# Optimization experiments

Measured on AMD Instinct MI355X. Metric: run time of the kernel, lower is better.

Reference implementation:

```python
import jax, jax.numpy as jnp
import numpy as np

B, M, N, L = 4096, 128, 96, 20


def setup_inputs() -> dict:
    key = jax.random.key(0)
    k1, k2, k3, k4 = jax.random.split(key, 4)
    x_ini = jax.random.normal(k1, (B, N, 1), jnp.float32)
    y = jax.random.normal(k2, (B, M, 1), jnp.float32)
    H = jax.random.normal(k3, (B, M, N), jnp.float32)
    xt = jax.random.normal(k4, (B, N, 1), jnp.float32)
    # learned parameters, initialized exactly as in the torch __init__
    grad_ss = jnp.full((L,), 0.001, jnp.float32)
    extra = []
    t = 1.0
    for _ in range(L):
        t1 = (1.0 + np.sqrt(1.0 + 4.0 * t * t)) / 2.0
        extra.append((t - 1.0) / t1)
        t = t1
    extra_ss = jnp.asarray(np.array(extra, dtype=np.float32))
    gamma1 = jnp.asarray(np.array([(5.0 - 0.1) / L * i + 0.1 for i in range(L)], dtype=np.float32))
    return {"x_ini": x_ini, "y": y, "H": H, "xt": xt,
            "grad_ss": grad_ss, "extra_ss": extra_ss, "gamma1": gamma1}


def reference(x_ini, y, H, xt, grad_ss, extra_ss, gamma1):
    central = jnp.array([-2.0, 0.0, 2.0], dtype=x_ini.dtype)  # 3-point codebook
    HTH = jnp.einsum('bmn,bmk->bnk', H, H)   # [B,N,N]
    HTy = jnp.einsum('bmn,bmk->bnk', H, y)   # [B,N,1]

    def step(carry, params):
        x, y_x = carry
        gs, es, gm = params
        grad_f = 2.0 * (jnp.matmul(HTH, y_x) - HTy)          # [B,N,1]
        x_buff = y_x - gs * grad_f                            # [B,N,1]
        # nearest-center lookup over the 3-entry codebook
        idx = jnp.argmin(jnp.abs(x_buff - central[None, None, :]), axis=2)  # [B,N]
        center = central[idx][..., None]                      # [B,N,1]
        ply = 2.0 * jax.nn.sigmoid(gm * (x_buff - center)) - 1.0
        y_x_new = ply + es * (ply - x)                        # FISTA momentum
        return (ply, y_x_new), None

    (x, _), _ = jax.lax.scan(step, (x_ini, x_ini), (grad_ss, extra_ss, gamma1))
    d = x - xt
    loss = jnp.sum(d * d).reshape(1, 1)  # sum_b (x-xt)^T (x-xt)
    return x, loss
```

## Files before the change

kernel.cpp:

```cpp
#include <hip/hip_runtime.h>

#define NB 4096
#define MM 128
#define NN 96
#define LL 20

typedef __attribute__((ext_vector_type(8))) short bf16x8;
typedef __attribute__((ext_vector_type(4))) float f32x4;
typedef __attribute__((ext_vector_type(4))) unsigned int u32x4;

#define HTP_STRIDE  67
#define HTHP_STRIDE 100
#define U_WORDS     (NN * HTHP_STRIDE)

#define SEL_HI 0x07060302u
#define SEL_LO 0x05040100u

__device__ __forceinline__ unsigned bf16_rne(float f) {
    unsigned u = __float_as_uint(f);
    return (u + 0x7fffu + ((u >> 16) & 1u)) >> 16;
}
__device__ __forceinline__ unsigned pack_hl(float v) {
    unsigned hi = bf16_rne(v);
    unsigned lo = bf16_rne(v - __uint_as_float(hi << 16));
    return (hi << 16) | (lo & 0xffffu);
}
__device__ __forceinline__ bf16x8 mk8(unsigned a, unsigned b, unsigned c, unsigned d) {
    u32x4 t; t[0] = a; t[1] = b; t[2] = c; t[3] = d;
    return __builtin_bit_cast(bf16x8, t);
}
struct PairHL { bf16x8 hi, lo; };
__device__ __forceinline__ PairHL build_pair(const unsigned q[8]) {
    PairHL p;
    p.hi = mk8(__builtin_amdgcn_perm(q[1], q[0], SEL_HI), __builtin_amdgcn_perm(q[3], q[2], SEL_HI),
               __builtin_amdgcn_perm(q[5], q[4], SEL_HI), __builtin_amdgcn_perm(q[7], q[6], SEL_HI));
    p.lo = mk8(__builtin_amdgcn_perm(q[1], q[0], SEL_LO), __builtin_amdgcn_perm(q[3], q[2], SEL_LO),
               __builtin_amdgcn_perm(q[5], q[4], SEL_LO), __builtin_amdgcn_perm(q[7], q[6], SEL_LO));
    return p;
}

__global__ __launch_bounds__(256) __attribute__((amdgpu_waves_per_eu(4)))
void pg_kernel(const float* __restrict__ x_ini,
               const float* __restrict__ y,
               const float* __restrict__ H,
               const float* __restrict__ xt,
               const float* __restrict__ grad_ss,
               const float* __restrict__ extra_ss,
               const float* __restrict__ gamma1,
               float* __restrict__ out)
{
    __shared__ __align__(16) unsigned U[U_WORDS];
    __shared__ __align__(16) unsigned yxP[NN];
    __shared__ __align__(16) float wbuf[NN];
    __shared__ float pgs[LL], pes[LL], pgm[LL];
    __shared__ float lsum[4];

    const int b    = blockIdx.x;
    const int tid  = threadIdx.x;
    const int lane = tid & 63;
    const int wid  = tid >> 6;
    const int m15  = lane & 15;
    const int g4   = lane >> 4;

    if (tid < LL) { pgs[tid] = grad_ss[tid]; pes[tid] = extra_ss[tid]; pgm[tid] = gamma1[tid]; }

    const int nJ = (wid == 3) ? 1 : 2;
    f32x4 acc[2][6];
    #pragma unroll
    for (int j = 0; j < 2; ++j)
        #pragma unroll
        for (int i = 0; i < 6; ++i)
            #pragma unroll
            for (int r = 0; r < 4; ++r) acc[j][i][r] = 0.f;

    const float* Hb = H + (size_t)b * (MM * NN);
    const int r16 = tid >> 2;
    const int cg4 = tid & 3;

    for (int kh = 0; kh < 2; ++kh) {
        if (kh) __syncthreads();
        {
            const float* src = Hb + (size_t)(kh * 64 + r16) * NN + cg4 * 24;
            float4 vv[6];
            #pragma unroll
            for (int i = 0; i < 6; ++i) vv[i] = *(const float4*)(src + 4 * i);
            #pragma unroll
            for (int i = 0; i < 6; ++i) {
                const int c = cg4 * 24 + 4 * i;
                U[(c + 0) * HTP_STRIDE + r16] = pack_hl(vv[i].x);
                U[(c + 1) * HTP_STRIDE + r16] = pack_hl(vv[i].y);
                U[(c + 2) * HTP_STRIDE + r16] = pack_hl(vv[i].z);
                U[(c + 3) * HTP_STRIDE + r16] = pack_hl(vv[i].w);
            }
            if (tid < 64)
                U[96 * HTP_STRIDE + tid] = pack_hl(y[(size_t)b * MM + kh * 64 + tid]);
        }
        __syncthreads();

        #pragma unroll
        for (int kk = 0; kk < 2; ++kk) {
            const int kbase = kk * 32 + g4 * 8;
            PairHL B[2];
            #pragma unroll
            for (int j = 0; j < 2; ++j) {
                if (j < nJ) {
                    const int J = wid + 4 * j;
                    unsigned q[8];
                    const unsigned* p = &U[(J * 16 + m15) * HTP_STRIDE + kbase];
                    #pragma unroll
                    for (int u = 0; u < 8; ++u) q[u] = p[u];
                    B[j] = build_pair(q);
                }
            }
            #pragma unroll
            for (int I = 0; I < 6; ++I) {
                unsigned q[8];
                const unsigned* p = &U[(I * 16 + m15) * HTP_STRIDE + kbase];
                #pragma unroll
                for (int u = 0; u < 8; ++u) q[u] = p[u];
                PairHL A = build_pair(q);
                #pragma unroll
                for (int j = 0; j < 2; ++j) {
                    if (j < nJ) {
                        acc[j][I] = __builtin_amdgcn_mfma_f32_16x16x32_bf16(A.hi, B[j].hi, acc[j][I], 0, 0, 0);
                        acc[j][I] = __builtin_amdgcn_mfma_f32_16x16x32_bf16(A.hi, B[j].lo, acc[j][I], 0, 0, 0);
                        acc[j][I] = __builtin_amdgcn_mfma_f32_16x16x32_bf16(A.lo, B[j].hi, acc[j][I], 0, 0, 0);
                    }
                }
            }
        }
    }
    __syncthreads();

    #pragma unroll
    for (int j = 0; j < 2; ++j) {
        if (j < nJ) {
            const int col = (wid + 4 * j) * 16 + m15;
            if (col <= 96) {
                #pragma unroll
                for (int I = 0; I < 6; ++I) {
                    const int rowb = I * 16 + g4 * 4;
                    #pragma unroll
                    for (int r = 0; r < 4; ++r)
                        U[(rowb + r) * HTHP_STRIDE + col] = pack_hl(acc[j][I][r]);
                }
            }
        }
    }
    __syncthreads();

    float yx_own = 0.f, x_c = 0.f, hty = 0.f;
    if (tid < NN) {
        yx_own = x_ini[(size_t)b * NN + tid];
        x_c    = yx_own;
        yxP[tid] = pack_hl(yx_own);
        unsigned p = U[tid * HTHP_STRIDE + 96];
        hty = __uint_as_float(p & 0xffff0000u) + __uint_as_float(p << 16);
    }
    const int nI = (wid < 2) ? 2 : 1;
    bf16x8 ahi[2][3], alo[2][3];
    #pragma unroll
    for (int t2 = 0; t2 < 2; ++t2) {
        if (t2 < nI) {
            const int I = wid + 4 * t2;
            #pragma unroll
            for (int kk = 0; kk < 3; ++kk) {
                unsigned q[8];
                const unsigned* p = &U[(I * 16 + m15) * HTHP_STRIDE + kk * 32 + g4 * 8];
                #pragma unroll
                for (int u = 0; u < 8; ++u) q[u] = p[u];
                PairHL A = build_pair(q);
                ahi[t2][kk] = A.hi;
                alo[t2][kk] = A.lo;
            }
        }
    }
    __syncthreads();

    for (int t = 0; t < LL; ++t) {
        bf16x8 bhi[3], blo[3];
        #pragma unroll
        for (int kk = 0; kk < 3; ++kk) {
            unsigned q[8];
            const unsigned* p = &yxP[kk * 32 + g4 * 8];
            #pragma unroll
            for (int u = 0; u < 8; ++u) q[u] = p[u];
            PairHL Bp = build_pair(q);
            bhi[kk] = Bp.hi; blo[kk] = Bp.lo;
        }
        f32x4 a0 = {0.f,0.f,0.f,0.f}, a1 = {0.f,0.f,0.f,0.f};
        #pragma unroll
        for (int kk = 0; kk < 3; ++kk) {
            a0 = __builtin_amdgcn_mfma_f32_16x16x32_bf16(ahi[0][kk], bhi[kk], a0, 0, 0, 0);
            a0 = __builtin_amdgcn_mfma_f32_16x16x32_bf16(ahi[0][kk], blo[kk], a0, 0, 0, 0);
            a0 = __builtin_amdgcn_mfma_f32_16x16x32_bf16(alo[0][kk], bhi[kk], a0, 0, 0, 0);
            if (1 < nI) {
                a1 = __builtin_amdgcn_mfma_f32_16x16x32_bf16(ahi[1][kk], bhi[kk], a1, 0, 0, 0);
                a1 = __builtin_amdgcn_mfma_f32_16x16x32_bf16(ahi[1][kk], blo[kk], a1, 0, 0, 0);
                a1 = __builtin_amdgcn_mfma_f32_16x16x32_bf16(alo[1][kk], bhi[kk], a1, 0, 0, 0);
            }
        }
        if (m15 == 0) {
            const int rb0 = wid * 16 + g4 * 4;
            wbuf[rb0 + 0] = a0[0]; wbuf[rb0 + 1] = a0[1];
            wbuf[rb0 + 2] = a0[2]; wbuf[rb0 + 3] = a0[3];
            if (1 < nI) {
                const int rb1 = (wid + 4) * 16 + g4 * 4;
                wbuf[rb1 + 0] = a1[0]; wbuf[rb1 + 1] = a1[1];
                wbuf[rb1 + 2] = a1[2]; wbuf[rb1 + 3] = a1[3];
            }
        }
        __syncthreads();

        if (tid < NN) {
            float w = wbuf[tid];
            const float gs = pgs[t], es = pes[t], gm = pgm[t];
            float xb  = fmaf(-2.0f * gs, w - hty, yx_own);
            float cen = 2.0f * fminf(fmaxf(rintf(xb * 0.5f), -1.0f), 1.0f);
            float z   = gm * (xb - cen);
            float e   = __expf(-z);
            float ply = fmaf(2.0f, __builtin_amdgcn_rcpf(1.0f + e), -1.0f);
            float yxn = fmaf(es, ply - x_c, ply);
            x_c    = ply;
            yx_own = yxn;
            yxP[tid] = pack_hl(yxn);
        }
        __syncthreads();
    }

    float part = 0.f;
    if (tid < NN) {
        out[(size_t)b * NN + tid] = x_c;
        float d = x_c - xt[(size_t)b * NN + tid];
        part = d * d;
    }
    #pragma unroll
    for (int m = 1; m < 64; m <<= 1) part += __shfl_xor(part, m, 64);
    if (lane == 0) lsum[wid] = part;
    __syncthreads();
    if (tid == 0) atomicAdd(out + (size_t)NB * NN, (lsum[0] + lsum[1]) + (lsum[2] + lsum[3]));
}

extern "C" void kernel_launch(void* const* d_in, const int* in_sizes, int n_in,
                              void* d_out, int out_size, void* d_ws, size_t ws_size,
                              hipStream_t stream) {
    const float* x_ini    = (const float*)d_in[0];
    const float* y        = (const float*)d_in[1];
    const float* H        = (const float*)d_in[2];
    const float* xt       = (const float*)d_in[3];
    const float* grad_ss  = (const float*)d_in[4];
    const float* extra_ss = (const float*)d_in[5];
    const float* gamma1   = (const float*)d_in[6];
    float* out = (float*)d_out;

    hipMemsetAsync(out + (size_t)NB * NN, 0, sizeof(float), stream);
    pg_kernel<<<NB, 256, 0, stream>>>(x_ini, y, H, xt, grad_ss, extra_ss, gamma1, out);
}
```

Measured before the change: 120.3 us.

## Split into HTH kernel and one-wave-per-batch FISTA kernel via workspace

Splits the fused kernel in two. The first kernel computes H^T H and H^T y and writes them to a global workspace in an MFMA-fragment layout. The second kernel runs the 20 FISTA iterations with one wave per batch item, so the per-iteration block-wide __syncthreads disappear and each wave holds the full HTH fragment set in registers. It also prefetches both H halves up front and uses vectorised LDS loads. The cost is extra global traffic through the workspace, possible chunked launches if the workspace is small, and higher register pressure in the FISTA kernel.

Result: slower. 170.8 us (+42.0%).

```diff
diff --git a/kernel.cpp b/kernel.cpp
--- a/kernel.cpp
+++ b/kernel.cpp
@@ -5,13 +5,12 @@
 #define NN 96
 #define LL 20
 
+#define SLOT_WORDS 9312
+#define HTP_STRIDE 68
+
 typedef __attribute__((ext_vector_type(8))) short bf16x8;
 typedef __attribute__((ext_vector_type(4))) float f32x4;
 typedef __attribute__((ext_vector_type(4))) unsigned int u32x4;
-
-#define HTP_STRIDE  67
-#define HTHP_STRIDE 100
-#define U_WORDS     (NN * HTHP_STRIDE)
 
 #define SEL_HI 0x07060302u
 #define SEL_LO 0x05040100u
@@ -30,41 +29,30 @@
     return __builtin_bit_cast(bf16x8, t);
 }
 struct PairHL { bf16x8 hi, lo; };
-__device__ __forceinline__ PairHL build_pair(const unsigned q[8]) {
+__device__ __forceinline__ PairHL unpack_pair(u32x4 q0, u32x4 q1) {
     PairHL p;
-    p.hi = mk8(__builtin_amdgcn_perm(q[1], q[0], SEL_HI), __builtin_amdgcn_perm(q[3], q[2], SEL_HI),
-               __builtin_amdgcn_perm(q[5], q[4], SEL_HI), __builtin_amdgcn_perm(q[7], q[6], SEL_HI));
-    p.lo = mk8(__builtin_amdgcn_perm(q[1], q[0], SEL_LO), __builtin_amdgcn_perm(q[3], q[2], SEL_LO),
-               __builtin_amdgcn_perm(q[5], q[4], SEL_LO), __builtin_amdgcn_perm(q[7], q[6], SEL_LO));
+    p.hi = mk8(__builtin_amdgcn_perm(q0[1], q0[0], SEL_HI), __builtin_amdgcn_perm(q0[3], q0[2], SEL_HI),
+               __builtin_amdgcn_perm(q1[1], q1[0], SEL_HI), __builtin_amdgcn_perm(q1[3], q1[2], SEL_HI));
+    p.lo = mk8(__builtin_amdgcn_perm(q0[1], q0[0], SEL_LO), __builtin_amdgcn_perm(q0[3], q0[2], SEL_LO),
+               __builtin_amdgcn_perm(q1[1], q1[0], SEL_LO), __builtin_amdgcn_perm(q1[3], q1[2], SEL_LO));
     return p;
 }
 
-__global__ __launch_bounds__(256) __attribute__((amdgpu_waves_per_eu(4)))
-void pg_kernel(const float* __restrict__ x_ini,
-               const float* __restrict__ y,
-               const float* __restrict__ H,
-               const float* __restrict__ xt,
-               const float* __restrict__ grad_ss,
-               const float* __restrict__ extra_ss,
-               const float* __restrict__ gamma1,
-               float* __restrict__ out)
+__global__ __launch_bounds__(256) __attribute__((amdgpu_waves_per_eu(3)))
+void hth_kernel(const float* __restrict__ H, const float* __restrict__ y,
+                unsigned* __restrict__ ws, int b0)
 {
-    __shared__ __align__(16) unsigned U[U_WORDS];
-    __shared__ __align__(16) unsigned yxP[NN];
-    __shared__ __align__(16) float wbuf[NN];
-    __shared__ float pgs[LL], pes[LL], pgm[LL];
-    __shared__ float lsum[4];
-
-    const int b    = blockIdx.x;
+    __shared__ unsigned U[112 * HTP_STRIDE];
+    const int b    = b0 + blockIdx.x;
     const int tid  = threadIdx.x;
     const int lane = tid & 63;
     const int wid  = tid >> 6;
     const int m15  = lane & 15;
     const int g4   = lane >> 4;
-
-    if (tid < LL) { pgs[tid] = grad_ss[tid]; pes[tid] = extra_ss[tid]; pgm[tid] = gamma1[tid]; }
-
-    const int nJ = (wid == 3) ? 1 : 2;
+    const int nJ   = (wid == 3) ? 1 : 2;
+    const int r16  = tid >> 2;
+    const int cg4  = tid & 3;
+
     f32x4 acc[2][6];
     #pragma unroll
     for (int j = 0; j < 2; ++j)
@@ -73,172 +61,203 @@
             #pragma unroll
             for (int r = 0; r < 4; ++r) acc[j][i][r] = 0.f;
 
-    const float* Hb = H + (size_t)b * (MM * NN);
-    const int r16 = tid >> 2;
-    const int cg4 = tid & 3;
+    const float* src = H + (size_t)b * (MM * NN) + (size_t)r16 * NN + cg4 * 24;
+    float4 v0[6], v1[6];
+    #pragma unroll
+    for (int i = 0; i < 6; ++i) {
+        v0[i] = *(const float4*)(src + 4 * i);
+        v1[i] = *(const float4*)(src + 64 * NN + 4 * i);
+    }
+    float ya = 0.f, yb = 0.f;
+    if (tid < 64) {
+        ya = y[(size_t)b * MM + tid];
+        yb = y[(size_t)b * MM + 64 + tid];
+    }
 
     for (int kh = 0; kh < 2; ++kh) {
         if (kh) __syncthreads();
-        {
-            const float* src = Hb + (size_t)(kh * 64 + r16) * NN + cg4 * 24;
-            float4 vv[6];
-            #pragma unroll
-            for (int i = 0; i < 6; ++i) vv[i] = *(const float4*)(src + 4 * i);
-            #pragma unroll
-            for (int i = 0; i < 6; ++i) {
-                const int c = cg4 * 24 + 4 * i;
-                U[(c + 0) * HTP_STRIDE + r16] = pack_hl(vv[i].x);
-                U[(c + 1) * HTP_STRIDE + r16] = pack_hl(vv[i].y);
-                U[(c + 2) * HTP_STRIDE + r16] = pack_hl(vv[i].z);
-                U[(c + 3) * HTP_STRIDE + r16] = pack_hl(vv[i].w);
-            }
-            if (tid < 64)
-                U[96 * HTP_STRIDE + tid] = pack_hl(y[(size_t)b * MM + kh * 64 + tid]);
-        }
+        #pragma unroll
+        for (int i = 0; i < 6; ++i) {
+            const float4 vv = kh ? v1[i] : v0[i];
+            const int c = cg4 * 24 + 4 * i;
+            U[(c + 0) * HTP_STRIDE + r16] = pack_hl(vv.x);
+            U[(c + 1) * HTP_STRIDE + r16] = pack_hl(vv.y);
+            U[(c + 2) * HTP_STRIDE + r16] = pack_hl(vv.z);
+            U[(c + 3) * HTP_STRIDE + r16] = pack_hl(vv.w);
+        }
+        if (tid < 64) U[96 * HTP_STRIDE + tid] = pack_hl(kh ? yb : ya);
         __syncthreads();
 
         #pragma unroll
         for (int kk = 0; kk < 2; ++kk) {
             const int kbase = kk * 32 + g4 * 8;
-            PairHL B[2];
+            bf16x8 Bh[2], Bl[2];
             #pragma unroll
             for (int j = 0; j < 2; ++j) {
                 if (j < nJ) {
-                    const int J = wid + 4 * j;
-                    unsigned q[8];
-                    const unsigned* p = &U[(J * 16 + m15) * HTP_STRIDE + kbase];
-                    #pragma unroll
-                    for (int u = 0; u < 8; ++u) q[u] = p[u];
-                    B[j] = build_pair(q);
+                    const int base = ((wid + 4 * j) * 16 + m15) * HTP_STRIDE + kbase;
+                    u32x4 q0 = *(const u32x4*)&U[base];
+                    u32x4 q1 = *(const u32x4*)&U[base + 4];
+                    PairHL p = unpack_pair(q0, q1);
+                    Bh[j] = p.hi; Bl[j] = p.lo;
                 }
             }
             #pragma unroll
             for (int I = 0; I < 6; ++I) {
-                unsigned q[8];
-                const unsigned* p = &U[(I * 16 + m15) * HTP_STRIDE + kbase];
-                #pragma unroll
-                for (int u = 0; u < 8; ++u) q[u] = p[u];
-                PairHL A = build_pair(q);
+                const int base = (I * 16 + m15) * HTP_STRIDE + kbase;
+                u32x4 q0 = *(const u32x4*)&U[base];
+                u32x4 q1 = *(const u32x4*)&U[base + 4];
+                PairHL A = unpack_pair(q0, q1);
                 #pragma unroll
                 for (int j = 0; j < 2; ++j) {
                     if (j < nJ) {
-                        acc[j][I] = __builtin_amdgcn_mfma_f32_16x16x32_bf16(A.hi, B[j].hi, acc[j][I], 0, 0, 0);
-                        acc[j][I] = __builtin_amdgcn_mfma_f32_16x16x32_bf16(A.hi, B[j].lo, acc[j][I], 0, 0, 0);
-                        acc[j][I] = __builtin_amdgcn_mfma_f32_16x16x32_bf16(A.lo, B[j].hi, acc[j][I], 0, 0, 0);
+                        acc[j][I] = __builtin_amdgcn_mfma_f32_16x16x32_bf16(A.hi, Bh[j], acc[j][I], 0, 0, 0);
+                        acc[j][I] = __builtin_amdgcn_mfma_f32_16x16x32_bf16(A.hi, Bl[j], acc[j][I], 0, 0, 0);
+                        acc[j][I] = __builtin_amdgcn_mfma_f32_16x16x32_bf16(A.lo, Bh[j], acc[j][I], 0, 0, 0);
                     }
                 }
             }
         }
     }
-    __syncthreads();
-
+
+    unsigned* slot = ws + (size_t)blockIdx.x * SLOT_WORDS;
+    float* htyp = (float*)(slot + 9216);
     #pragma unroll
     for (int j = 0; j < 2; ++j) {
         if (j < nJ) {
             const int col = (wid + 4 * j) * 16 + m15;
-            if (col <= 96) {
+            #pragma unroll
+            for (int I = 0; I < 6; ++I) {
                 #pragma unroll
-                for (int I = 0; I < 6; ++I) {
-                    const int rowb = I * 16 + g4 * 4;
-                    #pragma unroll
-                    for (int r = 0; r < 4; ++r)
-                        U[(rowb + r) * HTHP_STRIDE + col] = pack_hl(acc[j][I][r]);
+                for (int r = 0; r < 4; ++r) {
+                    const int row = I * 16 + g4 * 4 + r;
+                    if (col < 96) {
+                        const int w = ((I * 3 + (col >> 5)) * 64 + ((col >> 3) & 3) * 16 + (row & 15)) * 8 + (col & 7);
+                        slot[w] = pack_hl(acc[j][I][r]);
+                    } else if (col == 96) {
+                        htyp[row] = acc[j][I][r];
+                    }
                 }
             }
         }
     }
-    __syncthreads();
-
-    float yx_own = 0.f, x_c = 0.f, hty = 0.f;
-    if (tid < NN) {
-        yx_own = x_ini[(size_t)b * NN + tid];
-        x_c    = yx_own;
-        yxP[tid] = pack_hl(yx_own);
-        unsigned p = U[tid * HTHP_STRIDE + 96];
-        hty = __uint_as_float(p & 0xffff0000u) + __uint_as_float(p << 16);
-    }
-    const int nI = (wid < 2) ? 2 : 1;
-    bf16x8 ahi[2][3], alo[2][3];
-    #pragma unroll
-    for (int t2 = 0; t2 < 2; ++t2) {
-        if (t2 < nI) {
-            const int I = wid + 4 * t2;
-            #pragma unroll
-            for (int kk = 0; kk < 3; ++kk) {
-                unsigned q[8];
-                const unsigned* p = &U[(I * 16 + m15) * HTHP_STRIDE + kk * 32 + g4 * 8];
-                #pragma unroll
-                for (int u = 0; u < 8; ++u) q[u] = p[u];
-                PairHL A = build_pair(q);
-                ahi[t2][kk] = A.hi;
-                alo[t2][kk] = A.lo;
-            }
-        }
-    }
-    __syncthreads();
+}
+
+__global__ __launch_bounds__(256) __attribute__((amdgpu_waves_per_eu(2)))
+void fista_kernel(const unsigned* __restrict__ ws,
+                  const float* __restrict__ x_ini,
+                  const float* __restrict__ xt,
+                  const float* __restrict__ grad_ss,
+                  const float* __restrict__ extra_ss,
+                  const float* __restrict__ gamma1,
+                  float* __restrict__ out, int b0)
+{
+    __shared__ unsigned yxP[4][NN];
+    const int tid  = threadIdx.x;
+    const int lane = tid & 63;
+    const int wid  = tid >> 6;
+    const int m15  = lane & 15;
+    const int g4   = lane >> 4;
+    const int lb   = blockIdx.x * 4 + wid;
+    const int b    = b0 + lb;
+    const unsigned* slot = ws + (size_t)lb * SLOT_WORDS;
+
+    bf16x8 ahi[6][3], alo[6][3];
+    #pragma unroll
+    for (int I = 0; I < 6; ++I)
+        #pragma unroll
+        for (int kk = 0; kk < 3; ++kk) {
+            const u32x4* p = (const u32x4*)(slot + ((size_t)(I * 3 + kk) * 64 + lane) * 8);
+            PairHL A = unpack_pair(p[0], p[1]);
+            ahi[I][kk] = A.hi; alo[I][kk] = A.lo;
+        }
+
+    const int  rb = m15 * 16 + g4 * 4;
+    const bool wr = (m15 < 6);
+    float yx4[4] = {0,0,0,0}, xc4[4] = {0,0,0,0}, hty4[4] = {0,0,0,0};
+    if (wr) {
+        float4 xi = *(const float4*)(x_ini + (size_t)b * NN + rb);
+        float4 ht = *(const float4*)((const float*)(slot + 9216) + rb);
+        yx4[0] = xi.x; yx4[1] = xi.y; yx4[2] = xi.z; yx4[3] = xi.w;
+        xc4[0] = xi.x; xc4[1] = xi.y; xc4[2] = xi.z; xc4[3] = xi.w;
+        hty4[0] = ht.x; hty4[1] = ht.y; hty4[2] = ht.z; hty4[3] = ht.w;
+        u32x4 pk;
+        #pragma unroll
+        for (int r = 0; r < 4; ++r) pk[r] = pack_hl(yx4[r]);
+        *(u32x4*)&yxP[wid][rb] = pk;
+    }
+    __builtin_amdgcn_sched_barrier(0);
 
     for (int t = 0; t < LL; ++t) {
         bf16x8 bhi[3], blo[3];
         #pragma unroll
         for (int kk = 0; kk < 3; ++kk) {
-            unsigned q[8];
-            const unsigned* p = &yxP[kk * 32 + g4 * 8];
-            #pragma unroll
-            for (int u = 0; u < 8; ++u) q[u] = p[u];
-            PairHL Bp = build_pair(q);
-            bhi[kk] = Bp.hi; blo[kk] = Bp.lo;
-        }
-        f32x4 a0 = {0.f,0.f,0.f,0.f}, a1 = {0.f,0.f,0.f,0.f};
+            u32x4 q0 = *(const u32x4*)&yxP[wid][kk * 32 + g4 * 8];
+            u32x4 q1 = *(const u32x4*)&yxP[wid][kk * 32 + g4 * 8 + 4];
+            PairHL p = unpack_pair(q0, q1);
+            bhi[kk] = p.hi; blo[kk] = p.lo;
+        }
+        f32x4 a0 = {0,0,0,0}, a1 = {0,0,0,0}, a2 = {0,0,0,0}, a3 = {0,0,0,0}, a4 = {0,0,0,0}, a5 = {0,0,0,0};
         #pragma unroll
         for (int kk = 0; kk < 3; ++kk) {
             a0 = __builtin_amdgcn_mfma_f32_16x16x32_bf16(ahi[0][kk], bhi[kk], a0, 0, 0, 0);
             a0 = __builtin_amdgcn_mfma_f32_16x16x32_bf16(ahi[0][kk], blo[kk], a0, 0, 0, 0);
             a0 = __builtin_amdgcn_mfma_f32_16x16x32_bf16(alo[0][kk], bhi[kk], a0, 0, 0, 0);
-            if (1 < nI) {
-                a1 = __builtin_amdgcn_mfma_f32_16x16x32_bf16(ahi[1][kk], bhi[kk], a1, 0, 0, 0);
-                a1 = __builtin_amdgcn_mfma_f32_16x16x32_bf16(ahi[1][kk], blo[kk], a1, 0, 0, 0);
-                a1 = __builtin_amdgcn_mfma_f32_16x16x32_bf16(alo[1][kk], bhi[kk], a1, 0, 0, 0);
-            }
-        }
-        if (m15 == 0) {
-            const int rb0 = wid * 16 + g4 * 4;
-            wbuf[rb0 + 0] = a0[0]; wbuf[rb0 + 1] = a0[1];
-            wbuf[rb0 + 2] = a0[2]; wbuf[rb0 + 3] = a0[3];
-            if (1 < nI) {
-                const int rb1 = (wid + 4) * 16 + g4 * 4;
-                wbuf[rb1 + 0] = a1[0]; wbuf[rb1 + 1] = a1[1];
-                wbuf[rb1 + 2] = a1[2]; wbuf[rb1 + 3] = a1[3];
-            }
-        }
-        __syncthreads();
-
-        if (tid < NN) {
-            float w = wbuf[tid];
-            const float gs = pgs[t], es = pes[t], gm = pgm[t];
-            float xb  = fmaf(-2.0f * gs, w - hty, yx_own);
-            float cen = 2.0f * fminf(fmaxf(rintf(xb * 0.5f), -1.0f), 1.0f);
-            float z   = gm * (xb - cen);
-            float e   = __expf(-z);
-            float ply = fmaf(2.0f, __builtin_amdgcn_rcpf(1.0f + e), -1.0f);
-            float yxn = fmaf(es, ply - x_c, ply);
-            x_c    = ply;
-            yx_own = yxn;
-            yxP[tid] = pack_hl(yxn);
-        }
-        __syncthreads();
+            a1 = __builtin_amdgcn_mfma_f32_16x16x32_bf16(ahi[1][kk], bhi[kk], a1, 0, 0, 0);
+            a1 = __builtin_amdgcn_mfma_f32_16x16x32_bf16(ahi[1][kk], blo[kk], a1, 0, 0, 0);
+            a1 = __builtin_amdgcn_mfma_f32_16x16x32_bf16(alo[1][kk], bhi[kk], a1, 0, 0, 0);
+            a2 = __builtin_amdgcn_mfma_f32_16x16x32_bf16(ahi[2][kk], bhi[kk], a2, 0, 0, 0);
+            a2 = __builtin_amdgcn_mfma_f32_16x16x32_bf16(ahi[2][kk], blo[kk], a2, 0, 0, 0);
+            a2 = __builtin_amdgcn_mfma_f32_16x16x32_bf16(alo[2][kk], bhi[kk], a2, 0, 0, 0);
+            a3 = __builtin_amdgcn_mfma_f32_16x16x32_bf16(ahi[3][kk], bhi[kk], a3, 0, 0, 0);
+            a3 = __builtin_amdgcn_mfma_f32_16x16x32_bf16(ahi[3][kk], blo[kk], a3, 0, 0, 0);
+            a3 = __builtin_amdgcn_mfma_f32_16x16x32_bf16(alo[3][kk], bhi[kk], a3, 0, 0, 0);
+            a4 = __builtin_amdgcn_mfma_f32_16x16x32_bf16(ahi[4][kk], bhi[kk], a4, 0, 0, 0);
+            a4 = __builtin_amdgcn_mfma_f32_16x16x32_bf16(ahi[4][kk], blo[kk], a4, 0, 0, 0);
+            a4 = __builtin_amdgcn_mfma_f32_16x16x32_bf16(alo[4][kk], bhi[kk], a4, 0, 0, 0);
+            a5 = __builtin_amdgcn_mfma_f32_16x16x32_bf16(ahi[5][kk], bhi[kk], a5, 0, 0, 0);
+            a5 = __builtin_amdgcn_mfma_f32_16x16x32_bf16(ahi[5][kk], blo[kk], a5, 0, 0, 0);
+            a5 = __builtin_amdgcn_mfma_f32_16x16x32_bf16(alo[5][kk], bhi[kk], a5, 0, 0, 0);
+        }
+        f32x4 am = a0;
+        am = (m15 == 1) ? a1 : am;
+        am = (m15 == 2) ? a2 : am;
+        am = (m15 == 3) ? a3 : am;
+        am = (m15 == 4) ? a4 : am;
+        am = (m15 == 5) ? a5 : am;
+
+        const float gs = grad_ss[t], es = extra_ss[t], gm = gamma1[t];
+        if (wr) {
+            u32x4 pk;
+            #pragma unroll
+            for (int r = 0; r < 4; ++r) {
+                float xb  = fmaf(-2.0f * gs, am[r] - hty4[r], yx4[r]);
+                float cen = 2.0f * fminf(fmaxf(rintf(xb * 0.5f), -1.0f), 1.0f);
+                float z   = gm * (xb - cen);
+                float e   = __expf(-z);
+                float ply = fmaf(2.0f, __builtin_amdgcn_rcpf(1.0f + e), -1.0f);
+                float yxn = fmaf(es, ply - xc4[r], ply);
+                xc4[r] = ply;
+                yx4[r] = yxn;
+                pk[r]  = pack_hl(yxn);
+            }
+            if (t + 1 < LL) *(u32x4*)&yxP[wid][rb] = pk;
+        }
+        __builtin_amdgcn_sched_barrier(0);
     }
 
     float part = 0.f;
-    if (tid < NN) {
-        out[(size_t)b * NN + tid] = x_c;
-        float d = x_c - xt[(size_t)b * NN + tid];
-        part = d * d;
+    if (wr) {
+        float4 xo, xr;
+        xo.x = xc4[0]; xo.y = xc4[1]; xo.z = xc4[2]; xo.w = xc4[3];
+        *(float4*)(out + (size_t)b * NN + rb) = xo;
+        xr = *(const float4*)(xt + (size_t)b * NN + rb);
+        float d0 = xc4[0] - xr.x, d1 = xc4[1] - xr.y, d2 = xc4[2] - xr.z, d3 = xc4[3] - xr.w;
+        part = (d0 * d0 + d1 * d1) + (d2 * d2 + d3 * d3);
     }
     #pragma unroll
     for (int m = 1; m < 64; m <<= 1) part += __shfl_xor(part, m, 64);
-    if (lane == 0) lsum[wid] = part;
-    __syncthreads();
-    if (tid == 0) atomicAdd(out + (size_t)NB * NN, (lsum[0] + lsum[1]) + (lsum[2] + lsum[3]));
+    if (lane == 0) atomicAdd(out + (size_t)NB * NN, part);
 }
 
 extern "C" void kernel_launch(void* const* d_in, const int* in_sizes, int n_in,
@@ -252,7 +271,17 @@
     const float* extra_ss = (const float*)d_in[5];
     const float* gamma1   = (const float*)d_in[6];
     float* out = (float*)d_out;
+    unsigned* ws = (unsigned*)d_ws;
+
+    int CB = (int)(ws_size / (SLOT_WORDS * 4));
+    if (CB > NB) CB = NB;
+    CB &= ~3;
+    if (CB < 4) CB = 4;
 
     hipMemsetAsync(out + (size_t)NB * NN, 0, sizeof(float), stream);
-    pg_kernel<<<NB, 256, 0, stream>>>(x_ini, y, H, xt, grad_ss, extra_ss, gamma1, out);
-}
+    for (int b0 = 0; b0 < NB; b0 += CB) {
+        int n = NB - b0; if (n > CB) n = CB;
+        hth_kernel<<<n, 256, 0, stream>>>(H, y, ws, b0);
+        fista_kernel<<<n / 4, 256, 0, stream>>>(ws, x_ini, xt, grad_ss, extra_ss, gamma1, out, b0);
+    }
+}
```
